# Performance work log

Hardware: AMD Instinct MI355X
Metric: run time of the kernel (lower is better)

## Reference

```python
import jax, jax.numpy as jnp
import numpy as np

WORD = 512
ED = 64


def setup_inputs() -> dict:
    key = jax.random.key(0)
    ks = jax.random.split(key, 7)
    x = jax.random.normal(ks[0], (4, 4096, WORD), dtype=jnp.float32)
    # Dense layer params (kernel + bias) for query/key/value projections
    s = 1.0 / np.sqrt(WORD)
    Wq = jax.random.normal(ks[1], (WORD, ED), dtype=jnp.float32) * s
    Wk = jax.random.normal(ks[2], (WORD, ED), dtype=jnp.float32) * s
    Wv = jax.random.normal(ks[3], (WORD, ED), dtype=jnp.float32) * s
    bq = jnp.zeros((ED,), dtype=jnp.float32)
    bk = jnp.zeros((ED,), dtype=jnp.float32)
    bv = jnp.zeros((ED,), dtype=jnp.float32)
    return {"x": x, "Wq": Wq, "bq": bq, "Wk": Wk, "bk": bk, "Wv": Wv, "bv": bv}


def reference(x, Wq, bq, Wk, bk, Wv, bv):
    # Q, K, V: [B, S, ED]
    Q = jnp.einsum('bsw,we->bse', x, Wq) + bq
    K = jnp.einsum('bsw,we->bse', x, Wk) + bk
    V = jnp.einsum('bsw,we->bse', x, Wv) + bv
    scale = 1.0 / jnp.sqrt(jnp.float32(ED))
    score = jnp.einsum('bqe,bke->bqk', Q, K) * scale  # [B, S, S]
    attn = jax.nn.softmax(score, axis=-1)
    Z = jnp.einsum('bqk,bke->bqe', attn, V)  # [B, S, ED]
    return Z
```

## Files before the change

### kernel.cpp

```cpp
#include <hip/hip_runtime.h>
#include <cstdint>


typedef __bf16 bf16x8 __attribute__((ext_vector_type(8)));
typedef float f32x4 __attribute__((ext_vector_type(4)));
typedef float f32x16 __attribute__((ext_vector_type(16)));
typedef int i32x2 __attribute__((ext_vector_type(2)));

#define SCALEQ 0.18033688011112042f

#define WT_OFF 0u
#define Q_OFF  262144u
#define K_OFF  2359296u
#define VT_OFF 4456448u
#define L_OFF  6553600u
#define OP_OFF 7077888u

#if defined(__has_builtin)
#if __has_builtin(__builtin_amdgcn_permlane32_swap)
#define HAVE_PLSWAP 1
#endif
#endif
#ifndef HAVE_PLSWAP
#define HAVE_PLSWAP 0
#endif

__device__ __forceinline__ unsigned short bf16_1(float a) {
  unsigned ua = __builtin_bit_cast(unsigned, a);
  ua += 0x7FFFu + ((ua >> 16) & 1u);
  return (unsigned short)(ua >> 16);
}
__device__ __forceinline__ unsigned pk_bf16(float a, float b) {
  unsigned ua = __builtin_bit_cast(unsigned, a);
  unsigned ub = __builtin_bit_cast(unsigned, b);
  ua += 0x7FFFu + ((ua >> 16) & 1u);
  ub += 0x7FFFu + ((ub >> 16) & 1u);
  return (ua >> 16) | (ub & 0xFFFF0000u);
}
__device__ __forceinline__ unsigned pkru(float lo, float hi) {
  unsigned a = __builtin_bit_cast(unsigned, lo) + 0x8000u;
  unsigned b = __builtin_bit_cast(unsigned, hi) + 0x8000u;
  return __builtin_amdgcn_perm(b, a, 0x07060302u);
}
__device__ __forceinline__ void plswap(unsigned& x, unsigned& y, unsigned hl) {
#if HAVE_PLSWAP
  i32x2 r = __builtin_amdgcn_permlane32_swap((int)x, (int)y, false, false);
  x = (unsigned)r[0];
  y = (unsigned)r[1];
#else
  unsigned xs = (unsigned)__shfl_xor((int)x, 32);
  unsigned ys = (unsigned)__shfl_xor((int)y, 32);
  unsigned nx = hl ? ys : x;
  unsigned ny = hl ? y : xs;
  x = nx;
  y = ny;
#endif
}

__global__ __launch_bounds__(256) void prep_w(const float* __restrict__ Wq,
                                              const float* __restrict__ Wk,
                                              const float* __restrict__ Wv,
                                              unsigned short* __restrict__ wt2) {
  unsigned gtid = blockIdx.x * 256u + threadIdx.x;
  unsigned mat = gtid >> 15, rem = gtid & 32767u;
  const float* w = (mat == 0) ? Wq : (mat == 1) ? Wk : Wv;
  float v = w[rem];
  unsigned k = rem >> 6, n = rem & 63u;
  unsigned col = mat * 64u + n;
  unsigned ntg = col >> 4, l15c = col & 15u;
  unsigned kc = k >> 5, quad = (k >> 3) & 3u, j = k & 7u;
  wt2[((ntg * 16u + kc) * 64u + quad * 16u + l15c) * 8u + j] = bf16_1(v);
}

__global__ __launch_bounds__(256, 2) void qkv_proj(
    const float* __restrict__ x, const unsigned short* __restrict__ wt2,
    const float* __restrict__ bq, const float* __restrict__ bk,
    const float* __restrict__ bv, unsigned short* __restrict__ qws,
    unsigned short* __restrict__ kws, unsigned short* __restrict__ vtws) {
  __shared__ __align__(16) char xs[32768];
  __shared__ float biasl[192];
  const unsigned t = threadIdx.x;
  const unsigned row0 = blockIdx.x * 32u;
  const unsigned w = t >> 6, lane = t & 63u, l15 = lane & 15u, quad = lane >> 4;
  const unsigned rh = w & 1u, nh = w >> 1;

  if (t < 192u) {
    unsigned mat = t >> 6, n = t & 63u;
    biasl[t] = (mat == 0) ? bq[n] : (mat == 1) ? bk[n] : bv[n];
  }
#pragma unroll
  for (int i = 0; i < 16; i++) {
    unsigned idx4 = t + 256u * (unsigned)i;
    unsigned fidx = idx4 * 4u;
    unsigned row = fidx >> 9, k = fidx & 511u, g = k >> 3;
    float4 f = *(const float4*)(x + row0 * 512u + fidx);
    int2 v = make_int2(pkru(f.x, f.y), pkru(f.z, f.w));
    *(int2*)(xs + row * 1024u + ((g ^ (row & 7u)) << 4) + (k & 7u) * 2u) = v;
  }
  __syncthreads();

  f32x4 acc[6];
#pragma unroll
  for (int i = 0; i < 6; i++) acc[i] = {0.f, 0.f, 0.f, 0.f};
  const unsigned arow = rh * 16u + l15;
  const unsigned short* wbase = wt2 + (nh * 6144u + lane) * 8u;

  int4 cur[6], nxt[6];
#pragma unroll
  for (int nt = 0; nt < 6; nt++)
    cur[nt] = *(const int4*)(wbase + (unsigned)nt * 8192u);
  for (unsigned kc = 0; kc < 16u; kc++) {
    if (kc < 15u) {
#pragma unroll
      for (int nt = 0; nt < 6; nt++)
        nxt[nt] = *(const int4*)(wbase + ((unsigned)nt * 16u + kc + 1u) * 512u);
    }
    unsigned ag = kc * 4u + quad;
    int4 av = *(const int4*)(xs + arow * 1024u + ((ag ^ (arow & 7u)) << 4));
    bf16x8 a = __builtin_bit_cast(bf16x8, av);
#pragma unroll
    for (int nt = 0; nt < 6; nt++)
      acc[nt] = __builtin_amdgcn_mfma_f32_16x16x32_bf16(
          a, __builtin_bit_cast(bf16x8, cur[nt]), acc[nt], 0, 0, 0);
#pragma unroll
    for (int nt = 0; nt < 6; nt++) cur[nt] = nxt[nt];
  }
  unsigned sb = row0 + rh * 16u + quad * 4u;
  unsigned vb = sb >> 12, s = sb & 4095u;
#pragma unroll
  for (int nt = 0; nt < 6; nt++) {
    unsigned col = nh * 96u + (unsigned)nt * 16u + l15;
    unsigned mat = col >> 6, n = col & 63u;
    float bb = biasl[col];
    if (mat == 0) {
#pragma unroll
      for (int r = 0; r < 4; r++)
        qws[(sb + (unsigned)r) * 64u + n] = bf16_1((acc[nt][r] + bb) * SCALEQ);
    } else if (mat == 1) {
#pragma unroll
      for (int r = 0; r < 4; r++)
        kws[(sb + (unsigned)r) * 64u + n] = bf16_1(acc[nt][r] + bb);
    } else {
      int2 pv = make_int2(pk_bf16(acc[nt][0] + bb, acc[nt][1] + bb),
                          pk_bf16(acc[nt][2] + bb, acc[nt][3] + bb));
      *(int2*)(vtws + vb * 262144u + n * 4096u + s) = pv;
    }
  }
}

__global__ __launch_bounds__(256, 2) void attn(
    const unsigned short* __restrict__ qws, const unsigned short* __restrict__ kws,
    const unsigned short* __restrict__ vtws, float* __restrict__ lws,
    unsigned short* __restrict__ opp) {
  __shared__ __align__(16) char sm[34816];
  const unsigned t = threadIdx.x;
  const unsigned w = t >> 6, lane = t & 63u, l31 = lane & 31u, hl = lane >> 5;
  const unsigned bid = blockIdx.x;
  const unsigned ks = bid >> 6;
  const unsigned b = (bid >> 4) & 3u;
  const unsigned qt = bid & 15u;
  const unsigned q0 = qt * 256u + w * 64u;
  const unsigned key0 = ks * 512u;

  bf16x8 qf[2][4];
#pragma unroll
  for (int qt2 = 0; qt2 < 2; qt2++)
#pragma unroll
    for (int kq = 0; kq < 4; kq++)
      qf[qt2][kq] = __builtin_bit_cast(
          bf16x8,
          *(const int4*)(qws + (b * 4096u + q0 + (unsigned)qt2 * 32u + l31) * 64u +
                         (unsigned)kq * 16u + hl * 8u));
  f32x16 accO[2][2];
#pragma unroll
  for (int i = 0; i < 2; i++)
#pragma unroll
    for (int j = 0; j < 2; j++)
#pragma unroll
      for (int r = 0; r < 16; r++) accO[i][j][r] = 0.f;
  float lsum[2] = {0.f, 0.f};

  const unsigned short* kg = kws + (b * 4096u + key0) * 64u;
  const unsigned short* vg = vtws + b * 262144u + key0;
  const unsigned r0s = t >> 3, g0s = t & 7u;
  const unsigned r1s = (t + 256u) >> 3, g1s = t & 7u;

  int4 stg[4];
#define LOADTILE(kt)                                                          \
  {                                                                           \
    stg[0] = *(const int4*)(kg + ((kt) * 64u + r0s) * 64u + g0s * 8u);        \
    stg[1] = *(const int4*)(kg + ((kt) * 64u + r1s) * 64u + g1s * 8u);        \
    stg[2] = *(const int4*)(vg + r0s * 4096u + (kt) * 64u + g0s * 8u);        \
    stg[3] = *(const int4*)(vg + r1s * 4096u + (kt) * 64u + g1s * 8u);        \
  }
#define WRITETILE(bi)                                                         \
  {                                                                           \
    char* base = sm + (bi) * 16384u;                                          \
    *(int4*)(base + r0s * 128u + ((g0s ^ (r0s & 7u)) << 4)) = stg[0];         \
    *(int4*)(base + r1s * 128u + ((g1s ^ (r1s & 7u)) << 4)) = stg[1];         \
    *(int4*)(base + 8192u + r0s * 128u + ((g0s ^ (r0s & 7u)) << 4)) = stg[2]; \
    *(int4*)(base + 8192u + r1s * 128u + ((g1s ^ (r1s & 7u)) << 4)) = stg[3]; \
  }
  LOADTILE(0u);
  WRITETILE(0u);
  __syncthreads();

  for (unsigned kt = 0; kt < 8u; kt++) {
    if (kt < 7u) LOADTILE(kt + 1u);
    char* kb_ = sm + (kt & 1u) * 16384u;
    char* vb_ = kb_ + 8192u;
    bf16x8 kf[2][4], vf[2][4];
#pragma unroll
    for (int kh = 0; kh < 2; kh++)
#pragma unroll
      for (int kq = 0; kq < 4; kq++) {
        unsigned row = (unsigned)kh * 32u + l31;
        kf[kh][kq] = __builtin_bit_cast(
            bf16x8, *(const int4*)(kb_ + row * 128u +
                                   ((((unsigned)kq * 2u + hl) ^ (row & 7u)) << 4)));
      }
#pragma unroll
    for (int dh = 0; dh < 2; dh++)
#pragma unroll
      for (int kqg = 0; kqg < 4; kqg++) {
        unsigned row = (unsigned)dh * 32u + l31;
        vf[dh][kqg] = __builtin_bit_cast(
            bf16x8, *(const int4*)(vb_ + row * 128u +
                                   ((((unsigned)kqg * 2u + hl) ^ (row & 7u)) << 4)));
      }
#pragma unroll
    for (int qt2 = 0; qt2 < 2; qt2++) {
      f32x16 s0, s1;
#pragma unroll
      for (int r = 0; r < 16; r++) { s0[r] = 0.f; s1[r] = 0.f; }
#pragma unroll
      for (int kq = 0; kq < 4; kq++) {
        s0 = __builtin_amdgcn_mfma_f32_32x32x16_bf16(kf[0][kq], qf[qt2][kq], s0, 0, 0, 0);
        s1 = __builtin_amdgcn_mfma_f32_32x32x16_bf16(kf[1][kq], qf[qt2][kq], s1, 0, 0, 0);
      }
      float lp = 0.f;
#pragma unroll
      for (int r = 0; r < 16; r++) {
        s0[r] = __builtin_amdgcn_exp2f(s0[r]);
        lp += s0[r];
        s1[r] = __builtin_amdgcn_exp2f(s1[r]);
        lp += s1[r];
      }
      lsum[qt2] += lp;
      unsigned pk[2][8];
#pragma unroll
      for (int c = 0; c < 4; c++) {
        pk[0][2 * c] = pkru(s0[4 * c + 0], s0[4 * c + 1]);
        pk[0][2 * c + 1] = pkru(s0[4 * c + 2], s0[4 * c + 3]);
        pk[1][2 * c] = pkru(s1[4 * c + 0], s1[4 * c + 1]);
        pk[1][2 * c + 1] = pkru(s1[4 * c + 2], s1[4 * c + 3]);
      }
#pragma unroll
      for (int kqg = 0; kqg < 4; kqg++) {
        int kh = kqg >> 1, kqpl = kqg & 1;
        unsigned a0 = pk[kh][4 * kqpl + 0], a1 = pk[kh][4 * kqpl + 1];
        unsigned b0 = pk[kh][4 * kqpl + 2], b1 = pk[kh][4 * kqpl + 3];
        plswap(a0, b0, hl);
        plswap(a1, b1, hl);
        int4 fr = make_int4((int)a0, (int)a1, (int)b0, (int)b1);
        bf16x8 pf = __builtin_bit_cast(bf16x8, fr);
#pragma unroll
        for (int dh = 0; dh < 2; dh++)
          accO[qt2][dh] = __builtin_amdgcn_mfma_f32_32x32x16_bf16(
              vf[dh][kqg], pf, accO[qt2][dh], 0, 0, 0);
      }
    }
    if (kt < 7u) {
      __syncthreads();
      WRITETILE((kt + 1u) & 1u);
      __syncthreads();
    }
  }
  __syncthreads();
  float* sc = (float*)(sm + w * 8704u);
#pragma unroll
  for (int qt2 = 0; qt2 < 2; qt2++) {
    float lt = lsum[qt2] + __shfl_xor(lsum[qt2], 32);
    if (hl == 0u)
      lws[ks * 16384u + b * 4096u + q0 + (unsigned)qt2 * 32u + l31] = lt;
#pragma unroll
    for (int dh = 0; dh < 2; dh++)
#pragma unroll
      for (int r = 0; r < 16; r++) {
        unsigned d = (unsigned)dh * 32u + (unsigned)(r & 3) +
                     8u * (unsigned)(r >> 2) + 4u * hl;
        sc[l31 * 68u + d] = accO[qt2][dh][r];
      }
#pragma unroll
    for (int i = 0; i < 4; i++) {
      unsigned ql = (lane >> 3) + (unsigned)i * 8u;
      unsigned d0 = (lane & 7u) * 8u;
      float4 f0 = *(const float4*)(sc + ql * 68u + d0);
      float4 f1 = *(const float4*)(sc + ql * 68u + d0 + 4u);
      int4 pv = make_int4(pkru(f0.x, f0.y), pkru(f0.z, f0.w),
                          pkru(f1.x, f1.y), pkru(f1.z, f1.w));
      *(int4*)(opp + ks * 1048576u +
               (b * 4096u + q0 + (unsigned)qt2 * 32u + ql) * 64u + d0) = pv;
    }
  }
}

__global__ __launch_bounds__(256) void combine(const unsigned short* __restrict__ opp,
                                               const float* __restrict__ lws,
                                               float* __restrict__ out) {
#pragma unroll
  for (int ii = 0; ii < 2; ii++) {
    unsigned slot = blockIdx.x * 512u + threadIdx.x + 256u * (unsigned)ii;
    unsigned q = slot >> 4, c = (slot & 15u) * 4u;
    float l = 0.f;
#pragma unroll
    for (int s = 0; s < 8; s++) l += lws[(unsigned)s * 16384u + q];
    float inv = 1.0f / l;
    float4 r = make_float4(0.f, 0.f, 0.f, 0.f);
#pragma unroll
    for (int s = 0; s < 8; s++) {
      int2 pv = *(const int2*)(opp + (unsigned)s * 1048576u + q * 64u + c);
      r.x += __builtin_bit_cast(float, (unsigned)pv.x << 16);
      r.y += __builtin_bit_cast(float, (unsigned)pv.x & 0xFFFF0000u);
      r.z += __builtin_bit_cast(float, (unsigned)pv.y << 16);
      r.w += __builtin_bit_cast(float, (unsigned)pv.y & 0xFFFF0000u);
    }
    r.x *= inv; r.y *= inv; r.z *= inv; r.w *= inv;
    *(float4*)(out + q * 64u + c) = r;
  }
}

extern "C" void kernel_launch(void* const* d_in, const int* in_sizes, int n_in,
                              void* d_out, int out_size, void* d_ws,
                              size_t ws_size, hipStream_t stream) {
  const float* x = (const float*)d_in[0];
  const float* Wq = (const float*)d_in[1];
  const float* bq = (const float*)d_in[2];
  const float* Wk = (const float*)d_in[3];
  const float* bk = (const float*)d_in[4];
  const float* Wv = (const float*)d_in[5];
  const float* bv = (const float*)d_in[6];
  char* ws = (char*)d_ws;
  unsigned short* wt2 = (unsigned short*)(ws + WT_OFF);
  unsigned short* qb = (unsigned short*)(ws + Q_OFF);
  unsigned short* kb = (unsigned short*)(ws + K_OFF);
  unsigned short* vtb = (unsigned short*)(ws + VT_OFF);
  float* lp = (float*)(ws + L_OFF);
  unsigned short* opp = (unsigned short*)(ws + OP_OFF);
  float* outp = (float*)d_out;

  prep_w<<<384, 256, 0, stream>>>(Wq, Wk, Wv, wt2);
  qkv_proj<<<512, 256, 0, stream>>>(x, wt2, bq, bk, bv, qb, kb, vtb);
  attn<<<512, 256, 0, stream>>>(qb, kb, vtb, lp, opp);
  combine<<<512, 256, 0, stream>>>(opp, lp, outp);
}
```

Before: 131.3 us.

## Pre-tile K/V into fragment layout and stream via global_load_lds with smaller blocks

The projection kernel now writes K and V directly into a per-64-key tile layout that matches the MFMA fragment order. The attention kernel can then copy each tile linearly into LDS, using global_load_lds when available, with no XOR swizzle or register staging. Both kernels move to smaller blocks (16 rows for the projection, 32 queries per wave for attention) with doubled grids and higher occupancy bounds. Fragments are now read from LDS inside the compute loop rather than preloaded. The trade-off is less Q reuse per K/V tile load, so total K/V traffic roughly doubles, and the linear LDS layout may cause bank conflicts.

```diff
diff --git a/kernel.cpp b/kernel.cpp
--- a/kernel.cpp
+++ b/kernel.cpp
@@ -11,8 +11,7 @@
 
 #define WT_OFF 0u
 #define Q_OFF  262144u
-#define K_OFF  2359296u
-#define VT_OFF 4456448u
+#define KV_OFF 2359296u
 #define L_OFF  6553600u
 #define OP_OFF 7077888u
 
@@ -20,9 +19,15 @@
 #if __has_builtin(__builtin_amdgcn_permlane32_swap)
 #define HAVE_PLSWAP 1
 #endif
+#if __has_builtin(__builtin_amdgcn_global_load_lds)
+#define HAVE_GLL 1
+#endif
 #endif
 #ifndef HAVE_PLSWAP
 #define HAVE_PLSWAP 0
+#endif
+#ifndef HAVE_GLL
+#define HAVE_GLL 0
 #endif
 
 __device__ __forceinline__ unsigned short bf16_1(float a) {
@@ -56,6 +61,13 @@
   y = ny;
 #endif
 }
+#if HAVE_GLL
+__device__ __forceinline__ void gll16(const void* g, void* l) {
+  __builtin_amdgcn_global_load_lds(
+      (const __attribute__((address_space(1))) void*)g,
+      (__attribute__((address_space(3))) void*)l, 16, 0, 0);
+}
+#endif
 
 __global__ __launch_bounds__(256) void prep_w(const float* __restrict__ Wq,
                                               const float* __restrict__ Wk,
@@ -72,24 +84,23 @@
   wt2[((ntg * 16u + kc) * 64u + quad * 16u + l15c) * 8u + j] = bf16_1(v);
 }
 
-__global__ __launch_bounds__(256, 2) void qkv_proj(
+__global__ __launch_bounds__(256, 4) void qkv_proj(
     const float* __restrict__ x, const unsigned short* __restrict__ wt2,
     const float* __restrict__ bq, const float* __restrict__ bk,
     const float* __restrict__ bv, unsigned short* __restrict__ qws,
-    unsigned short* __restrict__ kws, unsigned short* __restrict__ vtws) {
-  __shared__ __align__(16) char xs[32768];
+    unsigned short* __restrict__ kvws) {
+  __shared__ __align__(16) char xs[16384];
   __shared__ float biasl[192];
   const unsigned t = threadIdx.x;
-  const unsigned row0 = blockIdx.x * 32u;
+  const unsigned row0 = blockIdx.x * 16u;
   const unsigned w = t >> 6, lane = t & 63u, l15 = lane & 15u, quad = lane >> 4;
-  const unsigned rh = w & 1u, nh = w >> 1;
 
   if (t < 192u) {
     unsigned mat = t >> 6, n = t & 63u;
     biasl[t] = (mat == 0) ? bq[n] : (mat == 1) ? bk[n] : bv[n];
   }
 #pragma unroll
-  for (int i = 0; i < 16; i++) {
+  for (int i = 0; i < 8; i++) {
     unsigned idx4 = t + 256u * (unsigned)i;
     unsigned fidx = idx4 * 4u;
     unsigned row = fidx >> 9, k = fidx & 511u, g = k >> 3;
@@ -99,37 +110,36 @@
   }
   __syncthreads();
 
-  f32x4 acc[6];
-#pragma unroll
-  for (int i = 0; i < 6; i++) acc[i] = {0.f, 0.f, 0.f, 0.f};
-  const unsigned arow = rh * 16u + l15;
-  const unsigned short* wbase = wt2 + (nh * 6144u + lane) * 8u;
-
-  int4 cur[6], nxt[6];
-#pragma unroll
-  for (int nt = 0; nt < 6; nt++)
+  f32x4 acc[3];
+#pragma unroll
+  for (int i = 0; i < 3; i++) acc[i] = {0.f, 0.f, 0.f, 0.f};
+  const unsigned arow = l15;
+  const unsigned short* wbase = wt2 + (w * 3u * 1024u + lane) * 8u;
+
+  int4 cur[3], nxt[3];
+#pragma unroll
+  for (int nt = 0; nt < 3; nt++)
     cur[nt] = *(const int4*)(wbase + (unsigned)nt * 8192u);
   for (unsigned kc = 0; kc < 16u; kc++) {
     if (kc < 15u) {
 #pragma unroll
-      for (int nt = 0; nt < 6; nt++)
+      for (int nt = 0; nt < 3; nt++)
         nxt[nt] = *(const int4*)(wbase + ((unsigned)nt * 16u + kc + 1u) * 512u);
     }
     unsigned ag = kc * 4u + quad;
     int4 av = *(const int4*)(xs + arow * 1024u + ((ag ^ (arow & 7u)) << 4));
     bf16x8 a = __builtin_bit_cast(bf16x8, av);
 #pragma unroll
-    for (int nt = 0; nt < 6; nt++)
+    for (int nt = 0; nt < 3; nt++)
       acc[nt] = __builtin_amdgcn_mfma_f32_16x16x32_bf16(
           a, __builtin_bit_cast(bf16x8, cur[nt]), acc[nt], 0, 0, 0);
 #pragma unroll
-    for (int nt = 0; nt < 6; nt++) cur[nt] = nxt[nt];
-  }
-  unsigned sb = row0 + rh * 16u + quad * 4u;
-  unsigned vb = sb >> 12, s = sb & 4095u;
-#pragma unroll
-  for (int nt = 0; nt < 6; nt++) {
-    unsigned col = nh * 96u + (unsigned)nt * 16u + l15;
+    for (int nt = 0; nt < 3; nt++) cur[nt] = nxt[nt];
+  }
+  unsigned sb = row0 + quad * 4u;
+#pragma unroll
+  for (int nt = 0; nt < 3; nt++) {
+    unsigned col = w * 48u + (unsigned)nt * 16u + l15;
     unsigned mat = col >> 6, n = col & 63u;
     float bb = biasl[col];
     if (mat == 0) {
@@ -138,170 +148,165 @@
         qws[(sb + (unsigned)r) * 64u + n] = bf16_1((acc[nt][r] + bb) * SCALEQ);
     } else if (mat == 1) {
 #pragma unroll
-      for (int r = 0; r < 4; r++)
-        kws[(sb + (unsigned)r) * 64u + n] = bf16_1(acc[nt][r] + bb);
+      for (int r = 0; r < 4; r++) {
+        unsigned s = sb + (unsigned)r;
+        unsigned bb2 = s >> 12, tile = (s & 4095u) >> 6, kap = s & 63u;
+        kvws[(bb2 * 64u + tile) * 8192u + (n >> 3) * 512u + kap * 8u + (n & 7u)] =
+            bf16_1(acc[nt][r] + bb);
+      }
     } else {
+      unsigned s = sb;
+      unsigned bb2 = s >> 12, tile = (s & 4095u) >> 6;
+      unsigned kg = (s & 63u) >> 3, j0 = s & 7u;
       int2 pv = make_int2(pk_bf16(acc[nt][0] + bb, acc[nt][1] + bb),
                           pk_bf16(acc[nt][2] + bb, acc[nt][3] + bb));
-      *(int2*)(vtws + vb * 262144u + n * 4096u + s) = pv;
-    }
-  }
-}
-
-__global__ __launch_bounds__(256, 2) void attn(
-    const unsigned short* __restrict__ qws, const unsigned short* __restrict__ kws,
-    const unsigned short* __restrict__ vtws, float* __restrict__ lws,
+      *(int2*)(kvws + (bb2 * 64u + tile) * 8192u + (8u + kg) * 512u + n * 8u +
+               j0) = pv;
+    }
+  }
+}
+
+__global__ __launch_bounds__(256, 4) void attn(
+    const unsigned short* __restrict__ qws,
+    const unsigned short* __restrict__ kvws, float* __restrict__ lws,
     unsigned short* __restrict__ opp) {
   __shared__ __align__(16) char sm[34816];
   const unsigned t = threadIdx.x;
   const unsigned w = t >> 6, lane = t & 63u, l31 = lane & 31u, hl = lane >> 5;
   const unsigned bid = blockIdx.x;
-  const unsigned ks = bid >> 6;
-  const unsigned b = (bid >> 4) & 3u;
-  const unsigned qt = bid & 15u;
-  const unsigned q0 = qt * 256u + w * 64u;
-  const unsigned key0 = ks * 512u;
-
-  bf16x8 qf[2][4];
-#pragma unroll
-  for (int qt2 = 0; qt2 < 2; qt2++)
-#pragma unroll
-    for (int kq = 0; kq < 4; kq++)
-      qf[qt2][kq] = __builtin_bit_cast(
-          bf16x8,
-          *(const int4*)(qws + (b * 4096u + q0 + (unsigned)qt2 * 32u + l31) * 64u +
-                         (unsigned)kq * 16u + hl * 8u));
-  f32x16 accO[2][2];
-#pragma unroll
-  for (int i = 0; i < 2; i++)
-#pragma unroll
-    for (int j = 0; j < 2; j++)
-#pragma unroll
-      for (int r = 0; r < 16; r++) accO[i][j][r] = 0.f;
-  float lsum[2] = {0.f, 0.f};
-
-  const unsigned short* kg = kws + (b * 4096u + key0) * 64u;
-  const unsigned short* vg = vtws + b * 262144u + key0;
-  const unsigned r0s = t >> 3, g0s = t & 7u;
-  const unsigned r1s = (t + 256u) >> 3, g1s = t & 7u;
-
+  const unsigned ks = bid >> 7;
+  const unsigned b = (bid >> 5) & 3u;
+  const unsigned qt = bid & 31u;
+  const unsigned q0 = qt * 128u + w * 32u;
+  const unsigned short* kvb = kvws + (b * 64u + ks * 8u) * 8192u + lane * 8u;
+
+  bf16x8 qf[4];
+#pragma unroll
+  for (int kq = 0; kq < 4; kq++)
+    qf[kq] = __builtin_bit_cast(
+        bf16x8, *(const int4*)(qws + (b * 4096u + q0 + l31) * 64u +
+                               (unsigned)kq * 16u + hl * 8u));
+  f32x16 accO[2];
+#pragma unroll
+  for (int dh = 0; dh < 2; dh++)
+#pragma unroll
+    for (int r = 0; r < 16; r++) accO[dh][r] = 0.f;
+  float lsum = 0.f;
+
+#if HAVE_GLL
+#define STAGE(kt_, bi_)                                                \
+  {                                                                    \
+    _Pragma("unroll") for (int i = 0; i < 4; i++) {                    \
+      unsigned c = (unsigned)i * 4u + w;                               \
+      gll16(kvb + (kt_)*8192u + c * 512u,                              \
+            sm + (bi_)*16384u + c * 1024u + (w * 0u));                 \
+    }                                                                  \
+  }
+  STAGE(0u, 0u);
+  __syncthreads();
+#else
   int4 stg[4];
-#define LOADTILE(kt)                                                          \
-  {                                                                           \
-    stg[0] = *(const int4*)(kg + ((kt) * 64u + r0s) * 64u + g0s * 8u);        \
-    stg[1] = *(const int4*)(kg + ((kt) * 64u + r1s) * 64u + g1s * 8u);        \
-    stg[2] = *(const int4*)(vg + r0s * 4096u + (kt) * 64u + g0s * 8u);        \
-    stg[3] = *(const int4*)(vg + r1s * 4096u + (kt) * 64u + g1s * 8u);        \
-  }
-#define WRITETILE(bi)                                                         \
-  {                                                                           \
-    char* base = sm + (bi) * 16384u;                                          \
-    *(int4*)(base + r0s * 128u + ((g0s ^ (r0s & 7u)) << 4)) = stg[0];         \
-    *(int4*)(base + r1s * 128u + ((g1s ^ (r1s & 7u)) << 4)) = stg[1];         \
-    *(int4*)(base + 8192u + r0s * 128u + ((g0s ^ (r0s & 7u)) << 4)) = stg[2]; \
-    *(int4*)(base + 8192u + r1s * 128u + ((g1s ^ (r1s & 7u)) << 4)) = stg[3]; \
-  }
-  LOADTILE(0u);
-  WRITETILE(0u);
+#define LOADT(kt_)                                                       \
+  {                                                                      \
+    _Pragma("unroll") for (int i = 0; i < 4; i++) stg[i] =               \
+        *(const int4*)(kvb + (kt_)*8192u + ((unsigned)i * 4u + w) * 512u); \
+  }
+#define WRITET(bi_)                                                       \
+  {                                                                       \
+    _Pragma("unroll") for (int i = 0; i < 4; i++)                         \
+        *(int4*)(sm + (bi_)*16384u + ((unsigned)i * 4u + w) * 1024u +     \
+                 lane * 16u - lane * 16u + lane * 16u) = stg[i];          \
+  }
+  LOADT(0u);
+  {
+#pragma unroll
+    for (int i = 0; i < 4; i++)
+      *(int4*)(sm + ((unsigned)i * 4u + w) * 1024u + lane * 16u) = stg[i];
+  }
   __syncthreads();
+#endif
 
   for (unsigned kt = 0; kt < 8u; kt++) {
-    if (kt < 7u) LOADTILE(kt + 1u);
-    char* kb_ = sm + (kt & 1u) * 16384u;
-    char* vb_ = kb_ + 8192u;
-    bf16x8 kf[2][4], vf[2][4];
-#pragma unroll
-    for (int kh = 0; kh < 2; kh++)
+#if HAVE_GLL
+    if (kt < 7u) STAGE(kt + 1u, (kt + 1u) & 1u);
+#else
+    if (kt < 7u) LOADT(kt + 1u);
+#endif
+    char* kb = sm + (kt & 1u) * 16384u;
+#pragma unroll
+    for (int kh = 0; kh < 2; kh++) {
+      f32x16 z;
+#pragma unroll
+      for (int r = 0; r < 16; r++) z[r] = 0.f;
 #pragma unroll
       for (int kq = 0; kq < 4; kq++) {
-        unsigned row = (unsigned)kh * 32u + l31;
-        kf[kh][kq] = __builtin_bit_cast(
-            bf16x8, *(const int4*)(kb_ + row * 128u +
-                                   ((((unsigned)kq * 2u + hl) ^ (row & 7u)) << 4)));
-      }
-#pragma unroll
-    for (int dh = 0; dh < 2; dh++)
-#pragma unroll
-      for (int kqg = 0; kqg < 4; kqg++) {
-        unsigned row = (unsigned)dh * 32u + l31;
-        vf[dh][kqg] = __builtin_bit_cast(
-            bf16x8, *(const int4*)(vb_ + row * 128u +
-                                   ((((unsigned)kqg * 2u + hl) ^ (row & 7u)) << 4)));
-      }
-#pragma unroll
-    for (int qt2 = 0; qt2 < 2; qt2++) {
-      f32x16 s0, s1;
-#pragma unroll
-      for (int r = 0; r < 16; r++) { s0[r] = 0.f; s1[r] = 0.f; }
-#pragma unroll
-      for (int kq = 0; kq < 4; kq++) {
-        s0 = __builtin_amdgcn_mfma_f32_32x32x16_bf16(kf[0][kq], qf[qt2][kq], s0, 0, 0, 0);
-        s1 = __builtin_amdgcn_mfma_f32_32x32x16_bf16(kf[1][kq], qf[qt2][kq], s1, 0, 0, 0);
+        int4 kfr = *(const int4*)(kb + (((unsigned)kq * 2u + hl) * 64u +
+                                        (unsigned)kh * 32u + l31) * 16u);
+        z = __builtin_amdgcn_mfma_f32_32x32x16_bf16(
+            __builtin_bit_cast(bf16x8, kfr), qf[kq], z, 0, 0, 0);
       }
       float lp = 0.f;
 #pragma unroll
       for (int r = 0; r < 16; r++) {
-        s0[r] = __builtin_amdgcn_exp2f(s0[r]);
-        lp += s0[r];
-        s1[r] = __builtin_amdgcn_exp2f(s1[r]);
-        lp += s1[r];
-      }
-      lsum[qt2] += lp;
-      unsigned pk[2][8];
-#pragma unroll
-      for (int c = 0; c < 4; c++) {
-        pk[0][2 * c] = pkru(s0[4 * c + 0], s0[4 * c + 1]);
-        pk[0][2 * c + 1] = pkru(s0[4 * c + 2], s0[4 * c + 3]);
-        pk[1][2 * c] = pkru(s1[4 * c + 0], s1[4 * c + 1]);
-        pk[1][2 * c + 1] = pkru(s1[4 * c + 2], s1[4 * c + 3]);
-      }
-#pragma unroll
-      for (int kqg = 0; kqg < 4; kqg++) {
-        int kh = kqg >> 1, kqpl = kqg & 1;
-        unsigned a0 = pk[kh][4 * kqpl + 0], a1 = pk[kh][4 * kqpl + 1];
-        unsigned b0 = pk[kh][4 * kqpl + 2], b1 = pk[kh][4 * kqpl + 3];
+        z[r] = __builtin_amdgcn_exp2f(z[r]);
+        lp += z[r];
+      }
+      lsum += lp;
+      unsigned pk8[8];
+#pragma unroll
+      for (int c2 = 0; c2 < 4; c2++) {
+        pk8[2 * c2] = pkru(z[4 * c2 + 0], z[4 * c2 + 1]);
+        pk8[2 * c2 + 1] = pkru(z[4 * c2 + 2], z[4 * c2 + 3]);
+      }
+#pragma unroll
+      for (int kqpl = 0; kqpl < 2; kqpl++) {
+        unsigned a0 = pk8[4 * kqpl + 0], a1 = pk8[4 * kqpl + 1];
+        unsigned b0 = pk8[4 * kqpl + 2], b1 = pk8[4 * kqpl + 3];
         plswap(a0, b0, hl);
         plswap(a1, b1, hl);
         int4 fr = make_int4((int)a0, (int)a1, (int)b0, (int)b1);
         bf16x8 pf = __builtin_bit_cast(bf16x8, fr);
-#pragma unroll
-        for (int dh = 0; dh < 2; dh++)
-          accO[qt2][dh] = __builtin_amdgcn_mfma_f32_32x32x16_bf16(
-              vf[dh][kqg], pf, accO[qt2][dh], 0, 0, 0);
-      }
-    }
+        unsigned kqg = (unsigned)kh * 2u + (unsigned)kqpl;
+#pragma unroll
+        for (int dh = 0; dh < 2; dh++) {
+          int4 vfr = *(const int4*)(kb + 8192u + ((kqg * 2u + hl) * 64u +
+                                                  (unsigned)dh * 32u + l31) * 16u);
+          accO[dh] = __builtin_amdgcn_mfma_f32_32x32x16_bf16(
+              __builtin_bit_cast(bf16x8, vfr), pf, accO[dh], 0, 0, 0);
+        }
+      }
+    }
+    __syncthreads();
+#if !HAVE_GLL
     if (kt < 7u) {
+#pragma unroll
+      for (int i = 0; i < 4; i++)
+        *(int4*)(sm + ((kt + 1u) & 1u) * 16384u +
+                 ((unsigned)i * 4u + w) * 1024u + lane * 16u) = stg[i];
       __syncthreads();
-      WRITETILE((kt + 1u) & 1u);
-      __syncthreads();
-    }
-  }
-  __syncthreads();
+    }
+#endif
+  }
+  float lt = lsum + __shfl_xor(lsum, 32);
+  if (hl == 0u) lws[ks * 16384u + b * 4096u + q0 + l31] = lt;
   float* sc = (float*)(sm + w * 8704u);
 #pragma unroll
-  for (int qt2 = 0; qt2 < 2; qt2++) {
-    float lt = lsum[qt2] + __shfl_xor(lsum[qt2], 32);
-    if (hl == 0u)
-      lws[ks * 16384u + b * 4096u + q0 + (unsigned)qt2 * 32u + l31] = lt;
-#pragma unroll
-    for (int dh = 0; dh < 2; dh++)
-#pragma unroll
-      for (int r = 0; r < 16; r++) {
-        unsigned d = (unsigned)dh * 32u + (unsigned)(r & 3) +
-                     8u * (unsigned)(r >> 2) + 4u * hl;
-        sc[l31 * 68u + d] = accO[qt2][dh][r];
-      }
-#pragma unroll
-    for (int i = 0; i < 4; i++) {
-      unsigned ql = (lane >> 3) + (unsigned)i * 8u;
-      unsigned d0 = (lane & 7u) * 8u;
-      float4 f0 = *(const float4*)(sc + ql * 68u + d0);
-      float4 f1 = *(const float4*)(sc + ql * 68u + d0 + 4u);
-      int4 pv = make_int4(pkru(f0.x, f0.y), pkru(f0.z, f0.w),
-                          pkru(f1.x, f1.y), pkru(f1.z, f1.w));
-      *(int4*)(opp + ks * 1048576u +
-               (b * 4096u + q0 + (unsigned)qt2 * 32u + ql) * 64u + d0) = pv;
-    }
+  for (int dh = 0; dh < 2; dh++)
+#pragma unroll
+    for (int r = 0; r < 16; r++) {
+      unsigned d = (unsigned)dh * 32u + (unsigned)(r & 3) +
+                   8u * (unsigned)(r >> 2) + 4u * hl;
+      sc[l31 * 68u + d] = accO[dh][r];
+    }
+#pragma unroll
+  for (int i = 0; i < 4; i++) {
+    unsigned ql = (lane >> 3) + (unsigned)i * 8u;
+    unsigned d0 = (lane & 7u) * 8u;
+    float4 f0 = *(const float4*)(sc + ql * 68u + d0);
+    float4 f1 = *(const float4*)(sc + ql * 68u + d0 + 4u);
+    int4 pv = make_int4(pkru(f0.x, f0.y), pkru(f0.z, f0.w),
+                        pkru(f1.x, f1.y), pkru(f1.z, f1.w));
+    *(int4*)(opp + ks * 1048576u + (b * 4096u + q0 + ql) * 64u + d0) = pv;
   }
 }
 
@@ -343,14 +348,13 @@
   char* ws = (char*)d_ws;
   unsigned short* wt2 = (unsigned short*)(ws + WT_OFF);
   unsigned short* qb = (unsigned short*)(ws + Q_OFF);
-  unsigned short* kb = (unsigned short*)(ws + K_OFF);
-  unsigned short* vtb = (unsigned short*)(ws + VT_OFF);
+  unsigned short* kvb = (unsigned short*)(ws + KV_OFF);
   float* lp = (float*)(ws + L_OFF);
   unsigned short* opp = (unsigned short*)(ws + OP_OFF);
   float* outp = (float*)d_out;
 
   prep_w<<<384, 256, 0, stream>>>(Wq, Wk, Wv, wt2);
-  qkv_proj<<<512, 256, 0, stream>>>(x, wt2, bq, bk, bv, qb, kb, vtb);
-  attn<<<512, 256, 0, stream>>>(qb, kb, vtb, lp, opp);
+  qkv_proj<<<1024, 256, 0, stream>>>(x, wt2, bq, bk, bv, qb, kvb);
+  attn<<<1024, 256, 0, stream>>>(qb, kvb, lp, opp);
   combine<<<512, 256, 0, stream>>>(opp, lp, outp);
 }
```

Result: faster. 127.8 us (-2.6%).
